# Performance work log

Measured on AMD Instinct MI355X. Metric: run time of the kernel, lower is better.

## Reference

```python
import jax, jax.numpy as jnp
import numpy as np

N, K = 8192, 64          # num pixels (b*h*w), proj_dim
C, M = 19, 10            # num_classes, num_prototype


def setup_inputs() -> dict:
    key = jax.random.key(0)
    k1, k2, k3 = jax.random.split(key, 3)
    x = jax.random.normal(k1, (N, K), dtype=jnp.float32)
    x_var = jax.random.uniform(k2, (N, K), dtype=jnp.float32)  # positive variances
    proto_mean = jax.random.normal(k3, (C, M, K), dtype=jnp.float32) * 0.02  # trunc_normal std=0.02
    proto_var = jnp.ones((C, M, K), dtype=jnp.float32)
    return {"x": x, "x_var": x_var, "proto_mean": proto_mean, "proto_var": proto_var}


def reference(x, x_var, proto_mean, proto_var):
    # MLS similarity: sim = -0.5 * mean_k[ (mu - x)^2 / (sig_x + sig_p) + log(sig_x + sig_p) ]
    pm = proto_mean[:, :, None, :]            # (c, m, 1, k)
    pv = proto_var[:, :, None, :]             # (c, m, 1, k)
    mean_diff = jnp.square(pm - x)            # (c, m, n, k) broadcast
    var_sum = x_var + pv                      # (c, m, n, k)
    sim = mean_diff / var_sum + jnp.log(var_sum)
    sim = -0.5 * jnp.mean(sim, axis=-1)       # (c, m, n)
    return jnp.transpose(sim, (2, 0, 1))      # (n, c, m) == permute(2, 0, 1)
```

## Files before the change

### kernel.cpp

```cpp
#include <hip/hip_runtime.h>

#define NROWS 8192
#define KDIM 64
#define CDIM 19
#define MDIM 10
#define CMDIM (CDIM * MDIM)
#define CM_PER_BLOCK 19
#define ROWS_PER_BLOCK 64
#define LDS_STRIDE 65

__global__ __launch_bounds__(256)
void probproto_kernel(const float* __restrict__ x,
                      const float* __restrict__ xv,
                      const float* __restrict__ pm,
                      const float* __restrict__ pv,
                      float* __restrict__ out)
{
    __shared__ float xs_t[KDIM * LDS_STRIDE];
    __shared__ float xvs_t[KDIM * LDS_STRIDE];

    const int t   = threadIdx.x;
    const int n0  = blockIdx.x * ROWS_PER_BLOCK;
    const int cm0 = blockIdx.y * CM_PER_BLOCK;

    const float4* x4  = (const float4*)(x  + (size_t)n0 * KDIM);
    const float4* xv4 = (const float4*)(xv + (size_t)n0 * KDIM);
    #pragma unroll
    for (int i = 0; i < 4; ++i) {
        int idx = t + 256 * i;
        int r   = idx >> 4;
        int c4  = idx & 15;
        float4 a = x4[idx];
        float4 b = xv4[idx];
        int k = c4 * 4;
        xs_t[(k + 0) * LDS_STRIDE + r] = a.x;
        xs_t[(k + 1) * LDS_STRIDE + r] = a.y;
        xs_t[(k + 2) * LDS_STRIDE + r] = a.z;
        xs_t[(k + 3) * LDS_STRIDE + r] = a.w;
        xvs_t[(k + 0) * LDS_STRIDE + r] = b.x;
        xvs_t[(k + 1) * LDS_STRIDE + r] = b.y;
        xvs_t[(k + 2) * LDS_STRIDE + r] = b.z;
        xvs_t[(k + 3) * LDS_STRIDE + r] = b.w;
    }
    __syncthreads();

    const int wave = __builtin_amdgcn_readfirstlane(t >> 6);
    const int lane = t & 63;
    const int n    = n0 + lane;

    const float4* __restrict__ pm4 = (const float4*)(pm + (size_t)cm0 * KDIM);
    const float4* __restrict__ pv4 = (const float4*)(pv + (size_t)cm0 * KDIM);

    float accQ[5] = {0.f, 0.f, 0.f, 0.f, 0.f};
    float accL[5] = {0.f, 0.f, 0.f, 0.f, 0.f};

    #pragma unroll
    for (int kc = 0; kc < 4; ++kc) {
        float xr[16], xvr[16];
        #pragma unroll
        for (int i = 0; i < 16; ++i) {
            xr[i]  = xs_t [(kc * 16 + i) * LDS_STRIDE + lane];
            xvr[i] = xvs_t[(kc * 16 + i) * LDS_STRIDE + lane];
        }
        #pragma unroll
        for (int j = 0; j < 5; ++j) {
            const int cmi = wave + 4 * j;
            if (cmi < CM_PER_BLOCK) {
                float q    = accQ[j];
                float prod = 1.0f;
                #pragma unroll
                for (int i4 = 0; i4 < 4; ++i4) {
                    const float4 pmv = pm4[cmi * 16 + kc * 4 + i4];
                    const float4 pvv = pv4[cmi * 16 + kc * 4 + i4];
                    float v, d;
                    v = xvr[i4 * 4 + 0] + pvv.x;  d = pmv.x - xr[i4 * 4 + 0];
                    q = fmaf(d * d, __builtin_amdgcn_rcpf(v), q);  prod *= v;
                    v = xvr[i4 * 4 + 1] + pvv.y;  d = pmv.y - xr[i4 * 4 + 1];
                    q = fmaf(d * d, __builtin_amdgcn_rcpf(v), q);  prod *= v;
                    v = xvr[i4 * 4 + 2] + pvv.z;  d = pmv.z - xr[i4 * 4 + 2];
                    q = fmaf(d * d, __builtin_amdgcn_rcpf(v), q);  prod *= v;
                    v = xvr[i4 * 4 + 3] + pvv.w;  d = pmv.w - xr[i4 * 4 + 3];
                    q = fmaf(d * d, __builtin_amdgcn_rcpf(v), q);  prod *= v;
                }
                accQ[j] = q;
                accL[j] += __log2f(prod);
            }
        }
    }

    #pragma unroll
    for (int j = 0; j < 5; ++j) {
        const int cmi = wave + 4 * j;
        if (cmi < CM_PER_BLOCK) {
            out[(size_t)n * CMDIM + cm0 + cmi] =
                -(accQ[j] + 0.69314718055994531f * accL[j]) * (1.0f / 128.0f);
        }
    }
}

extern "C" void kernel_launch(void* const* d_in, const int* in_sizes, int n_in,
                              void* d_out, int out_size, void* d_ws, size_t ws_size,
                              hipStream_t stream) {
    const float* x  = (const float*)d_in[0];
    const float* xv = (const float*)d_in[1];
    const float* pm = (const float*)d_in[2];
    const float* pv = (const float*)d_in[3];
    float* out = (float*)d_out;

    dim3 grid(NROWS / ROWS_PER_BLOCK, CMDIM / CM_PER_BLOCK);
    probproto_kernel<<<grid, 256, 0, stream>>>(x, xv, pm, pv, out);
}
```

Baseline: 90.38 us.

## Specialize unit prototype variance by expanding quadratic and precomputing per-row terms

Detects at runtime whether proto_var is all ones and, if so, rewrites the similarity as dot products of precomputed per-row terms (1/(1+xv), x/(1+xv)) with per-prototype terms (m^2, -2m), plus a per-row constant holding the x^2 and log terms. This removes the per-output reciprocal and log work, leaving two FMAs per element. A slow scalar fallback covers general variances. It adds an LDS buffer of prototype coefficients and a block-wide flag check.

```diff
diff --git a/kernel.cpp b/kernel.cpp
--- a/kernel.cpp
+++ b/kernel.cpp
@@ -7,7 +7,7 @@
 #define CMDIM (CDIM * MDIM)
 #define CM_PER_BLOCK 19
 #define ROWS_PER_BLOCK 64
-#define LDS_STRIDE 65
+#define RB_STRIDE 67
 
 __global__ __launch_bounds__(256)
 void probproto_kernel(const float* __restrict__ x,
@@ -16,12 +16,26 @@
                       const float* __restrict__ pv,
                       float* __restrict__ out)
 {
-    __shared__ float xs_t[KDIM * LDS_STRIDE];
-    __shared__ float xvs_t[KDIM * LDS_STRIDE];
+    __shared__ float2 rb_t[KDIM * RB_STRIDE];
+    __shared__ float2 gh[CM_PER_BLOCK * KDIM];
+    __shared__ float  Srow[ROWS_PER_BLOCK];
+    __shared__ int    badpv;
 
     const int t   = threadIdx.x;
     const int n0  = blockIdx.x * ROWS_PER_BLOCK;
     const int cm0 = blockIdx.y * CM_PER_BLOCK;
+
+    if (t == 0) badpv = 0;
+    __syncthreads();
+
+    int localbad = 0;
+    for (int idx = t; idx < CM_PER_BLOCK * KDIM; idx += 256) {
+        float m   = pm[(size_t)cm0 * KDIM + idx];
+        float pvv = pv[(size_t)cm0 * KDIM + idx];
+        localbad |= (pvv != 1.0f);
+        gh[idx] = make_float2(m * m, -2.0f * m);
+    }
+    if (localbad) atomicOr(&badpv, 1);
 
     const float4* x4  = (const float4*)(x  + (size_t)n0 * KDIM);
     const float4* xv4 = (const float4*)(xv + (size_t)n0 * KDIM);
@@ -31,16 +45,29 @@
         int r   = idx >> 4;
         int c4  = idx & 15;
         float4 a = x4[idx];
-        float4 b = xv4[idx];
-        int k = c4 * 4;
-        xs_t[(k + 0) * LDS_STRIDE + r] = a.x;
-        xs_t[(k + 1) * LDS_STRIDE + r] = a.y;
-        xs_t[(k + 2) * LDS_STRIDE + r] = a.z;
-        xs_t[(k + 3) * LDS_STRIDE + r] = a.w;
-        xvs_t[(k + 0) * LDS_STRIDE + r] = b.x;
-        xvs_t[(k + 1) * LDS_STRIDE + r] = b.y;
-        xvs_t[(k + 2) * LDS_STRIDE + r] = b.z;
-        xvs_t[(k + 3) * LDS_STRIDE + r] = b.w;
+        float4 w = xv4[idx];
+        float v0 = 1.0f + w.x, v1 = 1.0f + w.y, v2 = 1.0f + w.z, v3 = 1.0f + w.w;
+        float r0 = __builtin_amdgcn_rcpf(v0);
+        float r1 = __builtin_amdgcn_rcpf(v1);
+        float r2 = __builtin_amdgcn_rcpf(v2);
+        float r3 = __builtin_amdgcn_rcpf(v3);
+        float b0 = a.x * r0, b1 = a.y * r1, b2 = a.z * r2, b3 = a.w * r3;
+        int k0 = c4 * 4;
+        rb_t[(k0 + 0) * RB_STRIDE + r] = make_float2(r0, b0);
+        rb_t[(k0 + 1) * RB_STRIDE + r] = make_float2(r1, b1);
+        rb_t[(k0 + 2) * RB_STRIDE + r] = make_float2(r2, b2);
+        rb_t[(k0 + 3) * RB_STRIDE + r] = make_float2(r3, b3);
+        float e = a.x * b0;
+        e = fmaf(a.y, b1, e);
+        e = fmaf(a.z, b2, e);
+        e = fmaf(a.w, b3, e);
+        float prod = (v0 * v1) * (v2 * v3);
+        e = fmaf(0.69314718055994531f, __log2f(prod), e);
+        e += __shfl_xor(e, 1);
+        e += __shfl_xor(e, 2);
+        e += __shfl_xor(e, 4);
+        e += __shfl_xor(e, 8);
+        if ((t & 15) == 0) Srow[r] = e;
     }
     __syncthreads();
 
@@ -48,52 +75,55 @@
     const int lane = t & 63;
     const int n    = n0 + lane;
 
-    const float4* __restrict__ pm4 = (const float4*)(pm + (size_t)cm0 * KDIM);
-    const float4* __restrict__ pv4 = (const float4*)(pv + (size_t)cm0 * KDIM);
-
-    float accQ[5] = {0.f, 0.f, 0.f, 0.f, 0.f};
-    float accL[5] = {0.f, 0.f, 0.f, 0.f, 0.f};
-
-    #pragma unroll
-    for (int kc = 0; kc < 4; ++kc) {
-        float xr[16], xvr[16];
+    if (badpv == 0) {
+        float q[5] = {0.f, 0.f, 0.f, 0.f, 0.f};
         #pragma unroll
-        for (int i = 0; i < 16; ++i) {
-            xr[i]  = xs_t [(kc * 16 + i) * LDS_STRIDE + lane];
-            xvr[i] = xvs_t[(kc * 16 + i) * LDS_STRIDE + lane];
+        for (int kc = 0; kc < 4; ++kc) {
+            float rr[16], bb[16];
+            #pragma unroll
+            for (int i = 0; i < 16; ++i) {
+                float2 rb = rb_t[(kc * 16 + i) * RB_STRIDE + lane];
+                rr[i] = rb.x; bb[i] = rb.y;
+            }
+            #pragma unroll
+            for (int j = 0; j < 5; ++j) {
+                const int cmi = wave + 4 * j;
+                if (cmi < CM_PER_BLOCK) {
+                    float qq = q[j];
+                    #pragma unroll
+                    for (int i = 0; i < 16; ++i) {
+                        float2 c = gh[cmi * KDIM + kc * 16 + i];
+                        qq = fmaf(c.x, rr[i], qq);
+                        qq = fmaf(c.y, bb[i], qq);
+                    }
+                    q[j] = qq;
+                }
+            }
         }
+        const float S = Srow[lane];
         #pragma unroll
         for (int j = 0; j < 5; ++j) {
             const int cmi = wave + 4 * j;
             if (cmi < CM_PER_BLOCK) {
-                float q    = accQ[j];
-                float prod = 1.0f;
-                #pragma unroll
-                for (int i4 = 0; i4 < 4; ++i4) {
-                    const float4 pmv = pm4[cmi * 16 + kc * 4 + i4];
-                    const float4 pvv = pv4[cmi * 16 + kc * 4 + i4];
-                    float v, d;
-                    v = xvr[i4 * 4 + 0] + pvv.x;  d = pmv.x - xr[i4 * 4 + 0];
-                    q = fmaf(d * d, __builtin_amdgcn_rcpf(v), q);  prod *= v;
-                    v = xvr[i4 * 4 + 1] + pvv.y;  d = pmv.y - xr[i4 * 4 + 1];
-                    q = fmaf(d * d, __builtin_amdgcn_rcpf(v), q);  prod *= v;
-                    v = xvr[i4 * 4 + 2] + pvv.z;  d = pmv.z - xr[i4 * 4 + 2];
-                    q = fmaf(d * d, __builtin_amdgcn_rcpf(v), q);  prod *= v;
-                    v = xvr[i4 * 4 + 3] + pvv.w;  d = pmv.w - xr[i4 * 4 + 3];
-                    q = fmaf(d * d, __builtin_amdgcn_rcpf(v), q);  prod *= v;
-                }
-                accQ[j] = q;
-                accL[j] += __log2f(prod);
+                out[(size_t)n * CMDIM + cm0 + cmi] =
+                    -(q[j] + S) * (1.0f / 128.0f);
             }
         }
-    }
-
-    #pragma unroll
-    for (int j = 0; j < 5; ++j) {
-        const int cmi = wave + 4 * j;
-        if (cmi < CM_PER_BLOCK) {
+    } else {
+        const float* xrow  = x  + (size_t)n * KDIM;
+        const float* xvrow = xv + (size_t)n * KDIM;
+        for (int cmi = wave; cmi < CM_PER_BLOCK; cmi += 4) {
+            const float* pmrow = pm + (size_t)(cm0 + cmi) * KDIM;
+            const float* pvrow = pv + (size_t)(cm0 + cmi) * KDIM;
+            float accQ = 0.0f, accL = 0.0f;
+            for (int k = 0; k < KDIM; ++k) {
+                float v = xvrow[k] + pvrow[k];
+                float d = pmrow[k] - xrow[k];
+                accQ += d * d / v;
+                accL += __log2f(v);
+            }
             out[(size_t)n * CMDIM + cm0 + cmi] =
-                -(accQ[j] + 0.69314718055994531f * accL[j]) * (1.0f / 128.0f);
+                -(accQ + 0.69314718055994531f * accL) * (1.0f / 128.0f);
         }
     }
 }
```

Measured after the change: 82.82 us. 1.09x faster.
